# Performance work log

Measured on AMD Instinct MI355X. Metric: run time of the kernel, lower is better.

Reference implementation:

```python
import jax, jax.numpy as jnp
import numpy as np

NUM_DEP_TYPES = 53

def setup_inputs() -> dict:
    key = jax.random.key(0)
    k1, k2, k3, k4 = jax.random.split(key, 4)
    b, L = 128, 512
    dep_i = jax.random.randint(k1, (b, L - 1), 0, L)
    dep_j = jax.random.randint(k2, (b, L - 1), 0, L)
    dep_type = jax.random.randint(k3, (b, L - 1), 0, NUM_DEP_TYPES)
    dep_emb = jax.random.normal(k4, (NUM_DEP_TYPES, 1), dtype=jnp.float32)
    # padding_idx=0: row 0 of the embedding is zero
    dep_emb = dep_emb.at[0].set(0.0)
    return {"dep_i": dep_i, "dep_j": dep_j, "dep_type": dep_type,
            "seq_len": L, "dep_emb": dep_emb}

def reference(dep_i, dep_j, dep_type, seq_len, dep_emb):
    b = dep_i.shape[0]
    # start from all-ones [b, seq_len*seq_len] mask
    dep_mask = jnp.ones((b, seq_len * seq_len), dtype=dep_emb.dtype)
    dep_idx = dep_i * seq_len + dep_j                 # [b, seq_len-1]
    dep_k = dep_emb[dep_type, 0]                      # embedding gather -> [b, seq_len-1]
    rows = jnp.arange(b)[:, None]                     # broadcast row indices
    dep_mask = dep_mask.at[rows, dep_idx].set(dep_k)  # scatter along dim 1
    return dep_mask.reshape(b, seq_len, seq_len)
```

## Files before the change

### kernel.cpp

```cpp
#include <hip/hip_runtime.h>


#define SEQ_L   512
#define LM1     511
#define ROWELEM (SEQ_L * SEQ_L)
#define QUART   (ROWELEM / 4)
#define NT      256
#define HSLOTS  512
#define NEMBMAX 64

typedef float vfloat4 __attribute__((ext_vector_type(4)));

__device__ __forceinline__ unsigned hash_key(unsigned key) {
    return (key * 2654435761u) >> 23;
}

__global__ __launch_bounds__(NT) void depmask_fused(
    const int*   __restrict__ dep_i,
    const int*   __restrict__ dep_j,
    const int*   __restrict__ dep_type,
    const float* __restrict__ dep_emb,
    float*       __restrict__ out,
    int nemb)
{
    __shared__ int      h_key[HSLOTS];
    __shared__ unsigned h_pack[HSLOTS];
    __shared__ float    s_emb[NEMBMAX];

    const int b   = blockIdx.x;
    const int row = b >> 2;
    const int qtr = b & 3;
    const int t   = threadIdx.x;

    if (t < nemb) s_emb[t] = dep_emb[t];
    #pragma unroll
    for (int s = t; s < HSLOTS; s += NT) { h_key[s] = -1; h_pack[s] = 0; }

    const int base = row * LM1;
    const int k0 = t, k1 = t + NT;
    const int idx0 = dep_i[base + k0] * SEQ_L + dep_j[base + k0];
    const int ty0  = dep_type[base + k0];
    int idx1 = -1, ty1 = 0;
    if (k1 < LM1) {
        idx1 = dep_i[base + k1] * SEQ_L + dep_j[base + k1];
        ty1  = dep_type[base + k1];
    }

    __syncthreads();

    const float val0 = s_emb[ty0];
    const float val1 = (idx1 >= 0) ? s_emb[ty1] : 0.f;

    {
        const vfloat4 ones = {1.f, 1.f, 1.f, 1.f};
        vfloat4* o4 = reinterpret_cast<vfloat4*>(out)
                    + (size_t)row * (ROWELEM / 4) + (size_t)qtr * (QUART / 4);
        #pragma unroll 4
        for (int it = 0; it < QUART / 4 / NT; ++it)
            o4[it * NT + t] = ones;
    }

    if ((idx0 >> 16) == qtr) {
        const unsigned key = (unsigned)idx0 & 0xFFFFu;
        const unsigned pack = ((unsigned)k0 << 16) | key;
        unsigned s = hash_key(key);
        while (true) {
            int prev = atomicCAS(&h_key[s], -1, (int)key);
            if (prev == -1 || prev == (int)key) { atomicMax(&h_pack[s], pack); break; }
            s = (s + 1) & (HSLOTS - 1);
        }
    }
    if (idx1 >= 0 && (idx1 >> 16) == qtr) {
        const unsigned key = (unsigned)idx1 & 0xFFFFu;
        const unsigned pack = ((unsigned)k1 << 16) | key;
        unsigned s = hash_key(key);
        while (true) {
            int prev = atomicCAS(&h_key[s], -1, (int)key);
            if (prev == -1 || prev == (int)key) { atomicMax(&h_pack[s], pack); break; }
            s = (s + 1) & (HSLOTS - 1);
        }
    }

    __syncthreads();

    if ((idx0 >> 16) == qtr) {
        const unsigned key = (unsigned)idx0 & 0xFFFFu;
        const unsigned pack = ((unsigned)k0 << 16) | key;
        unsigned s = hash_key(key);
        while (h_key[s] != (int)key) s = (s + 1) & (HSLOTS - 1);
        if (h_pack[s] == pack) out[(size_t)row * ROWELEM + idx0] = val0;
    }
    if (idx1 >= 0 && (idx1 >> 16) == qtr) {
        const unsigned key = (unsigned)idx1 & 0xFFFFu;
        const unsigned pack = ((unsigned)k1 << 16) | key;
        unsigned s = hash_key(key);
        while (h_key[s] != (int)key) s = (s + 1) & (HSLOTS - 1);
        if (h_pack[s] == pack) out[(size_t)row * ROWELEM + idx1] = val1;
    }
}

extern "C" void kernel_launch(void* const* d_in, const int* in_sizes, int n_in,
                              void* d_out, int out_size, void* d_ws, size_t ws_size,
                              hipStream_t stream) {
    const int*   dep_i    = (const int*)  d_in[0];
    const int*   dep_j    = (const int*)  d_in[1];
    const int*   dep_type = (const int*)  d_in[2];
    const float* dep_emb  = (const float*)d_in[4];
    float*       out      = (float*)      d_out;

    const int rows = in_sizes[0] / LM1;
    const int nemb = in_sizes[4];

    depmask_fused<<<dim3(4 * rows), dim3(NT), 0, stream>>>(
        dep_i, dep_j, dep_type, dep_emb, out, nemb);
}
```

Before: 28.16 us.

## Write each output element once using shared-memory bitmap and hash value lookup

Instead of filling the quarter-row with ones and then scattering embedding values over them with separate global stores, the kernel builds a shared bitmap of occupied positions and stores the winning value per hash slot. The fill loop then checks the bitmap per float4 and substitutes hashed values inline, so each output element gets a single coalesced write. This removes the scattered second write pass but adds an extra barrier, an 8KB bitmap and a per-store bitmap read in the streaming loop.

```diff
diff --git a/kernel.cpp b/kernel.cpp
--- a/kernel.cpp
+++ b/kernel.cpp
@@ -8,6 +8,7 @@
 #define NT      256
 #define HSLOTS  512
 #define NEMBMAX 64
+#define BMWORDS (QUART / 32)
 
 typedef float vfloat4 __attribute__((ext_vector_type(4)));
 
@@ -15,7 +16,7 @@
     return (key * 2654435761u) >> 23;
 }
 
-__global__ __launch_bounds__(NT) void depmask_fused(
+__global__ __launch_bounds__(NT) void depmask_onewrite(
     const int*   __restrict__ dep_i,
     const int*   __restrict__ dep_j,
     const int*   __restrict__ dep_type,
@@ -23,8 +24,10 @@
     float*       __restrict__ out,
     int nemb)
 {
+    __shared__ unsigned bm[BMWORDS];
     __shared__ int      h_key[HSLOTS];
     __shared__ unsigned h_pack[HSLOTS];
+    __shared__ float    h_val[HSLOTS];
     __shared__ float    s_emb[NEMBMAX];
 
     const int b   = blockIdx.x;
@@ -33,6 +36,8 @@
     const int t   = threadIdx.x;
 
     if (t < nemb) s_emb[t] = dep_emb[t];
+    #pragma unroll
+    for (int w = t; w < BMWORDS; w += NT) bm[w] = 0u;
     #pragma unroll
     for (int s = t; s < HSLOTS; s += NT) { h_key[s] = -1; h_pack[s] = 0; }
 
@@ -45,57 +50,70 @@
         idx1 = dep_i[base + k1] * SEQ_L + dep_j[base + k1];
         ty1  = dep_type[base + k1];
     }
-
     __syncthreads();
 
     const float val0 = s_emb[ty0];
     const float val1 = (idx1 >= 0) ? s_emb[ty1] : 0.f;
+    const bool own0 = (idx0 >> 16) == qtr;
+    const bool own1 = idx1 >= 0 && ((idx1 >> 16) == qtr);
+    const unsigned key0 = (unsigned)idx0 & 0xFFFFu;
+    const unsigned key1 = (unsigned)idx1 & 0xFFFFu;
+    const unsigned pk0  = ((unsigned)k0 << 16) | key0;
+    const unsigned pk1  = ((unsigned)k1 << 16) | key1;
 
-    {
-        const vfloat4 ones = {1.f, 1.f, 1.f, 1.f};
-        vfloat4* o4 = reinterpret_cast<vfloat4*>(out)
-                    + (size_t)row * (ROWELEM / 4) + (size_t)qtr * (QUART / 4);
-        #pragma unroll 4
-        for (int it = 0; it < QUART / 4 / NT; ++it)
-            o4[it * NT + t] = ones;
-    }
-
-    if ((idx0 >> 16) == qtr) {
-        const unsigned key = (unsigned)idx0 & 0xFFFFu;
-        const unsigned pack = ((unsigned)k0 << 16) | key;
-        unsigned s = hash_key(key);
+    if (own0) {
+        unsigned s = hash_key(key0);
         while (true) {
-            int prev = atomicCAS(&h_key[s], -1, (int)key);
-            if (prev == -1 || prev == (int)key) { atomicMax(&h_pack[s], pack); break; }
+            int prev = atomicCAS(&h_key[s], -1, (int)key0);
+            if (prev == -1 || prev == (int)key0) { atomicMax(&h_pack[s], pk0); break; }
             s = (s + 1) & (HSLOTS - 1);
         }
+        atomicOr(&bm[key0 >> 5], 1u << (key0 & 31u));
     }
-    if (idx1 >= 0 && (idx1 >> 16) == qtr) {
-        const unsigned key = (unsigned)idx1 & 0xFFFFu;
-        const unsigned pack = ((unsigned)k1 << 16) | key;
-        unsigned s = hash_key(key);
+    if (own1) {
+        unsigned s = hash_key(key1);
         while (true) {
-            int prev = atomicCAS(&h_key[s], -1, (int)key);
-            if (prev == -1 || prev == (int)key) { atomicMax(&h_pack[s], pack); break; }
+            int prev = atomicCAS(&h_key[s], -1, (int)key1);
+            if (prev == -1 || prev == (int)key1) { atomicMax(&h_pack[s], pk1); break; }
             s = (s + 1) & (HSLOTS - 1);
         }
+        atomicOr(&bm[key1 >> 5], 1u << (key1 & 31u));
     }
-
     __syncthreads();
 
-    if ((idx0 >> 16) == qtr) {
-        const unsigned key = (unsigned)idx0 & 0xFFFFu;
-        const unsigned pack = ((unsigned)k0 << 16) | key;
-        unsigned s = hash_key(key);
-        while (h_key[s] != (int)key) s = (s + 1) & (HSLOTS - 1);
-        if (h_pack[s] == pack) out[(size_t)row * ROWELEM + idx0] = val0;
+    if (own0) {
+        unsigned s = hash_key(key0);
+        while (h_key[s] != (int)key0) s = (s + 1) & (HSLOTS - 1);
+        if (h_pack[s] == pk0) h_val[s] = val0;
     }
-    if (idx1 >= 0 && (idx1 >> 16) == qtr) {
-        const unsigned key = (unsigned)idx1 & 0xFFFFu;
-        const unsigned pack = ((unsigned)k1 << 16) | key;
-        unsigned s = hash_key(key);
-        while (h_key[s] != (int)key) s = (s + 1) & (HSLOTS - 1);
-        if (h_pack[s] == pack) out[(size_t)row * ROWELEM + idx1] = val1;
+    if (own1) {
+        unsigned s = hash_key(key1);
+        while (h_key[s] != (int)key1) s = (s + 1) & (HSLOTS - 1);
+        if (h_pack[s] == pk1) h_val[s] = val1;
+    }
+    __syncthreads();
+
+    vfloat4* o4 = reinterpret_cast<vfloat4*>(out)
+                + (size_t)row * (ROWELEM / 4) + (size_t)qtr * (QUART / 4);
+    const vfloat4 ones = {1.f, 1.f, 1.f, 1.f};
+    #pragma unroll 4
+    for (int it = 0; it < QUART / 4 / NT; ++it) {
+        const unsigned wbits = bm[it * 32 + (t >> 3)];
+        const unsigned nib = (wbits >> (4 * (t & 7))) & 0xFu;
+        vfloat4 v = ones;
+        if (nib) {
+            const unsigned cbase = (unsigned)(it * 1024 + 4 * t);
+            #pragma unroll
+            for (int j = 0; j < 4; ++j) {
+                if (nib & (1u << j)) {
+                    const unsigned key = cbase + j;
+                    unsigned s = hash_key(key);
+                    while (h_key[s] != (int)key) s = (s + 1) & (HSLOTS - 1);
+                    v[j] = h_val[s];
+                }
+            }
+        }
+        o4[it * NT + t] = v;
     }
 }
 
@@ -111,6 +129,6 @@
     const int rows = in_sizes[0] / LM1;
     const int nemb = in_sizes[4];
 
-    depmask_fused<<<dim3(4 * rows), dim3(NT), 0, stream>>>(
+    depmask_onewrite<<<dim3(4 * rows), dim3(NT), 0, stream>>>(
         dep_i, dep_j, dep_type, dep_emb, out, nemb);
 }
```

New measurement: 29.60 us. 5.1% more time.
